# Kernel tuning notes

Measured on AMD Instinct MI355X. Metric: run time of the kernel, lower is better.

## Reference

```python
import jax, jax.numpy as jnp
import numpy as np

B, N, K, H, F_IN = 16, 2048, 8, 128, 4  # graphs, nodes/graph, knn k, hidden, input feats


def _lin(key, fi, fo):
    s = 1.0 / np.sqrt(fi)
    kw, kb = jax.random.split(key)
    W = jax.random.uniform(kw, (fi, fo), jnp.float32, -s, s)
    b = jax.random.uniform(kb, (fo,), jnp.float32, -s, s)
    return W, b


def setup_inputs() -> dict:
    key = jax.random.key(0)
    ks = jax.random.split(key, 10)
    x = jax.random.normal(ks[0], (B * N, F_IN), jnp.float32)
    edge_index = jax.random.randint(ks[1], (2, B * N * K), 0, B * N, jnp.int64)  # unused by forward
    batch = jnp.repeat(jnp.arange(B, dtype=jnp.int64), N)
    W_enc, b_enc = _lin(ks[2], F_IN, H)
    W1a, b1a = _lin(ks[3], 2 * H, H)
    W1b, b1b = _lin(ks[4], H, H)
    W2a, b2a = _lin(ks[5], 2 * H, H)
    W2b, b2b = _lin(ks[6], H, H)
    W5a, b5a = _lin(ks[7], 2 * H, H)
    W5b, b5b = _lin(ks[8], H, 1)
    return dict(x=x, edge_index=edge_index, batch=batch,
                W_enc=W_enc, b_enc=b_enc,
                W1a=W1a, b1a=b1a, W1b=W1b, b1b=b1b,
                W2a=W2a, b2a=b2a, W2b=W2b, b2b=b2b,
                W5a=W5a, b5a=b5a, W5b=W5b, b5b=b5b)


def _knn(xb):
    # xb: [N, H] -> [N, K] indices of k nearest neighbors (self included, as in torch_cluster.knn)
    sq = jnp.sum(xb * xb, axis=-1)
    d = sq[:, None] + sq[None, :] - 2.0 * (xb @ xb.T)  # squared distances [N, N]
    return jax.lax.top_k(-d, K)[1]


def _edge_conv(x, Wa, ba, Wb, bb):
    # DynamicEdgeConv: rebuild kNN on current features, message = MLP([x_i, x_j - x_i]), max-aggregate.
    idx = jax.vmap(_knn)(x)                                   # [B, N, K]
    xj = jax.vmap(lambda xb, ib: xb[ib])(x, idx)              # [B, N, K, Hin]
    xi = jnp.broadcast_to(x[:, :, None, :], xj.shape)
    e = jnp.concatenate([xi, xj - xi], axis=-1)               # [B, N, K, 2*Hin]
    h = jax.nn.relu(e @ Wa + ba)                              # MLP applies ReLU after each Linear
    h = jax.nn.relu(h @ Wb + bb)
    return jnp.max(h, axis=2)                                 # max aggregation over neighbors


def reference(x, edge_index, batch, W_enc, b_enc,
              W1a, b1a, W1b, b1b, W2a, b2a, W2b, b2b, W5a, b5a, W5b, b5b):
    # batch is contiguous equal-size graphs -> reshape; edge_index is ignored by the original forward.
    h = x.reshape(B, N, F_IN) @ W_enc + b_enc
    h = jax.nn.relu(_edge_conv(h, W1a, b1a, W1b, b1b))
    h = jax.nn.relu(_edge_conv(h, W2a, b2a, W2b, b2b))
    out = jax.nn.sigmoid(_edge_conv(h, W5a, b5a, W5b, b5b))   # note: last MLP layer also has ReLU
    return out.reshape(B * N, 1)
```

## Files before the change

### kernel.cpp

```cpp
#include <hip/hip_runtime.h>
#include <hip/hip_bf16.h>
#include <math.h>

#define BGR 16
#define NPG 2048
#define HD  128
#define KNN 8
#define NTOT (BGR*NPG)

using bf16x8 = __attribute__((ext_vector_type(8))) short;
using f32x4  = __attribute__((ext_vector_type(4))) float;
using f32x16 = __attribute__((ext_vector_type(16))) float;

typedef __attribute__((address_space(3))) unsigned int lds_uint;
typedef const __attribute__((address_space(1))) unsigned int glob_uint;
#define GLOAD_LDS16(g, l) __builtin_amdgcn_global_load_lds((glob_uint*)(g), (lds_uint*)(l), 16, 0, 0)

__device__ inline unsigned short bf16rn(float f) {
    unsigned u = __float_as_uint(f);
    unsigned r = (u + 0x7FFFu + ((u >> 16) & 1u)) >> 16;
    return (unsigned short)r;
}
__device__ inline float bf16tof(unsigned short h) {
    return __uint_as_float(((unsigned)h) << 16);
}

__device__ inline void wcat_body(const float* __restrict__ Wa,
                                 unsigned short* __restrict__ Wt, int lb, int t)
{
    int gid = lb * 256 + t;
    int k = gid >> 8, n = gid & 255;
    float w;
    if (n < 128) w = Wa[(128 + k) * 128 + n];
    else { int nn = n - 128; w = Wa[k * 128 + nn] - Wa[(128 + k) * 128 + nn]; }
    unsigned short b1 = bf16rn(w);  float r1 = w - bf16tof(b1);
    unsigned short b2 = bf16rn(r1);
    int cs = n >> 5, h = (n >> 4) & 1, c = n & 15, kc = k >> 5, kg = (k >> 3) & 3, e = k & 7;
    size_t off = (size_t)cs * 12288 + kc * 1024 + h * 512 + kg * 128 + c * 8 + e;
    Wt[off] = b1; Wt[off + 4096] = b2;
}

__device__ inline void wb_body(const float* __restrict__ Wb,
                               unsigned short* __restrict__ Wt, int lb, int t)
{
    int gid = lb * 256 + t;
    int k = gid >> 7, n = gid & 127;
    float w = Wb[k * 128 + n];
    unsigned short b1 = bf16rn(w);  float r1 = w - bf16tof(b1);
    unsigned short b2 = bf16rn(r1);
    int cs = n >> 5, h = (n >> 4) & 1, c = n & 15, kc = k >> 5, kg = (k >> 3) & 3, e = k & 7;
    size_t off = (size_t)cs * 12288 + kc * 1024 + h * 512 + kg * 128 + c * 8 + e;
    Wt[off] = b1; Wt[off + 4096] = b2;
}

__global__ __launch_bounds__(256) void setup_all(const float* __restrict__ x,
                                                 const float* __restrict__ We,
                                                 const float* __restrict__ be,
                                                 unsigned short* __restrict__ hs,
                                                 float* __restrict__ sqg,
                                                 const float* __restrict__ W1a,
                                                 const float* __restrict__ W2a,
                                                 const float* __restrict__ W5a,
                                                 const float* __restrict__ W1b,
                                                 const float* __restrict__ W2b,
                                                 unsigned short* __restrict__ Wt1,
                                                 unsigned short* __restrict__ Wt2,
                                                 unsigned short* __restrict__ Wt5,
                                                 unsigned short* __restrict__ Wbt1,
                                                 unsigned short* __restrict__ Wbt2)
{
    const int bb = blockIdx.x, t = threadIdx.x;
    if (bb < 8192) {
        const size_t plane = (size_t)NTOT * HD;
        int node = (bb * 256 + t) >> 6;
        int lane = t & 63;
        float4 xv = *(const float4*)(x + (size_t)node * 4);
        float v0 = be[lane], v1 = be[lane + 64];
        const float* xf = (const float*)&xv;
#pragma unroll
        for (int f = 0; f < 4; ++f) {
            v0 = fmaf(xf[f], We[f * 128 + lane], v0);
            v1 = fmaf(xf[f], We[f * 128 + lane + 64], v1);
        }
        float s = fmaf(v0, v0, v1 * v1);
#pragma unroll
        for (int off = 32; off >= 1; off >>= 1)
            s += __shfl_xor(s, off);
        if (lane == 0) sqg[node] = s;
#pragma unroll
        for (int q = 0; q < 2; ++q) {
            float v = q ? v1 : v0;
            int   d = lane + q * 64;
            unsigned short b1 = bf16rn(v);  float r1 = v - bf16tof(b1);
            unsigned short b2 = bf16rn(r1);
            size_t base = (size_t)node * HD + d;
            hs[base]         = b1;
            hs[base + plane] = b2;
        }
    }
    else if (bb < 8320) wcat_body(W1a, Wt1, bb - 8192, t);
    else if (bb < 8448) wcat_body(W2a, Wt2, bb - 8320, t);
    else if (bb < 8576) wcat_body(W5a, Wt5, bb - 8448, t);
    else if (bb < 8640) wb_body(W1b, Wbt1, bb - 8576, t);
    else                wb_body(W2b, Wbt2, bb - 8640, t);
}

#define THREEPASS(B00,B01,B10,B11) \
    acc0 = __builtin_amdgcn_mfma_f32_16x16x32_bf16(A0[kc], B00, acc0, 0, 0, 0); \
    acc1 = __builtin_amdgcn_mfma_f32_16x16x32_bf16(A0[kc], B01, acc1, 0, 0, 0); \
    acc0 = __builtin_amdgcn_mfma_f32_16x16x32_bf16(A1[kc], B00, acc0, 0, 0, 0); \
    acc1 = __builtin_amdgcn_mfma_f32_16x16x32_bf16(A1[kc], B01, acc1, 0, 0, 0); \
    acc0 = __builtin_amdgcn_mfma_f32_16x16x32_bf16(A0[kc], B10, acc0, 0, 0, 0); \
    acc1 = __builtin_amdgcn_mfma_f32_16x16x32_bf16(A0[kc], B11, acc1, 0, 0, 0);

#define THREEPASS_G(AA0,AA1,B00,B01,B10,B11,C0,C1) \
    C0 = __builtin_amdgcn_mfma_f32_16x16x32_bf16(AA0[kc], B00, C0, 0, 0, 0); \
    C1 = __builtin_amdgcn_mfma_f32_16x16x32_bf16(AA0[kc], B01, C1, 0, 0, 0); \
    C0 = __builtin_amdgcn_mfma_f32_16x16x32_bf16(AA1[kc], B00, C0, 0, 0, 0); \
    C1 = __builtin_amdgcn_mfma_f32_16x16x32_bf16(AA1[kc], B01, C1, 0, 0, 0); \
    C0 = __builtin_amdgcn_mfma_f32_16x16x32_bf16(AA0[kc], B10, C0, 0, 0, 0); \
    C1 = __builtin_amdgcn_mfma_f32_16x16x32_bf16(AA0[kc], B11, C1, 0, 0, 0);

#define SELECT(PA, PB, PS) { \
    const unsigned lidbase = (unsigned)((PS) << 4); \
    _Pragma("unroll") \
    for (int i = 0; i < 16; ++i) { \
        float dsum = (PA)[i] + (PB)[i]; \
        unsigned ku = (__float_as_uint(dsum) & 0xFFFFFF00u) \
                    | (lidbase + (unsigned)i); \
        float kk = __uint_as_float(ku); \
        bd[7] = __builtin_amdgcn_fmed3f(bd[6], kk, bd[7]); \
        bd[6] = __builtin_amdgcn_fmed3f(bd[5], kk, bd[6]); \
        bd[5] = __builtin_amdgcn_fmed3f(bd[4], kk, bd[5]); \
        bd[4] = __builtin_amdgcn_fmed3f(bd[3], kk, bd[4]); \
        bd[3] = __builtin_amdgcn_fmed3f(bd[2], kk, bd[3]); \
        bd[2] = __builtin_amdgcn_fmed3f(bd[1], kk, bd[2]); \
        bd[1] = __builtin_amdgcn_fmed3f(bd[0], kk, bd[1]); \
        bd[0] = fminf(bd[0], kk); \
    } }

#define KNN_MFMA_STEP(ACCA, ACCB, S) { \
    const float* qq = sqs + (S) * 32 + kh * 4; \
    f32x4 q0 = *(const f32x4*)(qq); \
    f32x4 q1 = *(const f32x4*)(qq + 8); \
    f32x4 q2 = *(const f32x4*)(qq + 16); \
    f32x4 q3 = *(const f32x4*)(qq + 24); \
    ACCA[0]=q0[0]; ACCA[1]=q0[1]; ACCA[2]=q0[2]; ACCA[3]=q0[3]; \
    ACCA[4]=q1[0]; ACCA[5]=q1[1]; ACCA[6]=q1[2]; ACCA[7]=q1[3]; \
    ACCA[8]=q2[0]; ACCA[9]=q2[1]; ACCA[10]=q2[2]; ACCA[11]=q2[3]; \
    ACCA[12]=q3[0]; ACCA[13]=q3[1]; ACCA[14]=q3[2]; ACCA[15]=q3[3]; \
    ACCB = (f32x16){0.f,0.f,0.f,0.f,0.f,0.f,0.f,0.f,0.f,0.f,0.f,0.f,0.f,0.f,0.f,0.f}; \
    const char* pstep = ldsc + cur * 16384 + lane * 16; \
    __builtin_amdgcn_s_setprio(1); \
    _Pragma("unroll") \
    for (int kch = 0; kch < 8; ++kch) { \
        bf16x8 c0 = *(const bf16x8*)(pstep + kch * 1024); \
        bf16x8 c1 = *(const bf16x8*)(pstep + 8192 + kch * 1024); \
        ACCA = __builtin_amdgcn_mfma_f32_32x32x16_bf16(c0, RB[0][kch], ACCA, 0, 0, 0); \
        ACCB = __builtin_amdgcn_mfma_f32_32x32x16_bf16(c1, RB[0][kch], ACCB, 0, 0, 0); \
        if (kch & 1) ACCA = __builtin_amdgcn_mfma_f32_32x32x16_bf16(c0, RB[1][kch], ACCA, 0, 0, 0); \
        else         ACCB = __builtin_amdgcn_mfma_f32_32x32x16_bf16(c0, RB[1][kch], ACCB, 0, 0, 0); \
    } \
    __builtin_amdgcn_s_setprio(0); }

__global__ __launch_bounds__(256, 3) void knn_node(const unsigned short* __restrict__ hs,
                                                   const float* __restrict__ sqg,
                                                   const unsigned short* __restrict__ Wt,
                                                   const float* __restrict__ ba,
                                                   float* __restrict__ P,
                                                   float* __restrict__ D,
                                                   float* __restrict__ cand_d)
{
    __shared__ ulong2 ldsraw[2176];
    char* ldsc = (char*)ldsraw;
    const size_t plane = (size_t)NTOT * HD;
    const int t = threadIdx.x;
    const int wv = t >> 6, lane = t & 63;

    if (blockIdx.x < 512) {
        const int lrow = lane & 15, kg = lane >> 4;
        const int nodebase = blockIdx.x * 64 + wv * 16;

        const unsigned short* arow = hs + (size_t)(nodebase + lrow) * HD + kg * 8;
        bf16x8 A0[4], A1[4];
#pragma unroll
        for (int kc = 0; kc < 4; ++kc) {
            A0[kc] = *(const bf16x8*)(arow + kc * 32);
            A1[kc] = *(const bf16x8*)(arow + plane + kc * 32);
        }

        char* ldsw = ldsc + wv * 1024;
        const unsigned short* wsrc = Wt + t * 8;
#pragma unroll
        for (int i = 0; i < 4; ++i)
            GLOAD_LDS16(wsrc + i * 2048, ldsw + i * 4096);
        __syncthreads();

        int cur = 0;
        for (int cs = 0; cs < 8; ++cs) {
            if (cs < 7) {
#pragma unroll
                for (int i = 0; i < 4; ++i)
                    GLOAD_LDS16(wsrc + (size_t)(cs + 1) * 12288 + i * 2048,
                                ldsc + (cur ^ 1) * 16384 + wv * 1024 + i * 4096);
            }
            const char* pb = ldsc + cur * 16384 + kg * 256 + lrow * 16;
            f32x4 acc0 = {0.f,0.f,0.f,0.f};
            f32x4 acc1 = {0.f,0.f,0.f,0.f};
#pragma unroll
            for (int kc = 0; kc < 4; ++kc) {
                const char* pk = pb + kc * 2048;
                bf16x8 b00 = *(const bf16x8*)(pk);
                bf16x8 b01 = *(const bf16x8*)(pk + 1024);
                bf16x8 b10 = *(const bf16x8*)(pk + 8192);
                bf16x8 b11 = *(const bf16x8*)(pk + 9216);
                THREEPASS(b00, b01, b10, b11)
            }
            int n0 = cs * 32 + lrow;
            if (cs < 4) {
#pragma unroll
                for (int r = 0; r < 4; ++r) {
                    size_t row = (size_t)(nodebase + kg * 4 + r) * HD;
                    P[row + n0]      = acc0[r];
                    P[row + n0 + 16] = acc1[r];
                }
            } else {
                float ba0 = ba[n0 - 128], ba1 = ba[n0 - 112];
#pragma unroll
                for (int r = 0; r < 4; ++r) {
                    size_t row = (size_t)(nodebase + kg * 4 + r) * HD;
                    D[row + n0 - 128] = acc0[r] + ba0;
                    D[row + n0 - 112] = acc1[r] + ba1;
                }
            }
            __syncthreads();
            cur ^= 1;
        }
        return;
    }

    float* sqs = (float*)(ldsc + 32768);
    const int b = blockIdx.x - 512;
    const int slot = b >> 3;
    const int g  = (b & 7) | ((slot & 1) << 3);
    const int rb = (slot >> 1) & 15;
    const int cs = (slot >> 5) & 3;
    const int gbase = g * NPG;
    const int cbase = cs * 512;
    const int rl = lane & 31, kh = lane >> 5;
    const int myrow = rb * 128 + wv * 32 + rl;

    sqs[t]       = sqg[gbase + cbase + t];
    sqs[t + 256] = sqg[gbase + cbase + 256 + t];

    bf16x8 RB[2][8];
    {
        const unsigned short* rrow = hs + (size_t)(gbase + myrow) * HD + kh * 8;
#pragma unroll
        for (int p = 0; p < 2; ++p)
#pragma unroll
            for (int kch = 0; kch < 8; ++kch) {
                bf16x8 v = *(const bf16x8*)(rrow + (size_t)p * plane + kch * 16);
                unsigned* u = (unsigned*)&v;
#pragma unroll
                for (int w = 0; w < 4; ++w)
                    u[w] = (u[w] + 0x00800080u) ^ 0x80008000u;
                RB[p][kch] = v;
            }
    }

    const unsigned short* sb = hs + (size_t)(gbase + cbase + (t & 31)) * HD
                             + (t >> 6) * 16 + ((t >> 5) & 1) * 8;

#pragma unroll
    for (int i = 0; i < 4; ++i)
        GLOAD_LDS16(sb + (size_t)(i >> 1) * plane + (i & 1) * 64,
                    ldsc + wv * 1024 + i * 4096);
    __syncthreads();

    const float INF = __uint_as_float(0x7F800000u);
    float bd[8];
#pragma unroll
    for (int s = 0; s < 8; ++s) bd[s] = INF;

    f32x16 accA, accB;
    int cur = 0;
    for (int s = 0; s < 16; ++s) {
        if (s < 15) {
            const unsigned short* sbn = sb + (size_t)(s + 1) * 32 * HD;
#pragma unroll
            for (int i = 0; i < 4; ++i)
                GLOAD_LDS16(sbn + (size_t)(i >> 1) * plane + (i & 1) * 64,
                            ldsc + (cur ^ 1) * 16384 + wv * 1024 + i * 4096);
        }
        KNN_MFMA_STEP(accA, accB, s)
        SELECT(accA, accB, s)
        __syncthreads();
        cur ^= 1;
    }

    const size_t ob = (size_t)(gbase + myrow) * 64 + cs * 16 + kh * 8;
    f32x4 o0, o1;
#pragma unroll
    for (int sel = 0; sel < 8; ++sel) {
        unsigned u = __float_as_uint(bd[sel]);
        unsigned lid = u & 255u;
        unsigned j = (unsigned)(cbase + (int)(lid >> 4) * 32 + (int)((lid >> 2) & 3u) * 8
                              + kh * 4 + (int)(lid & 3u));
        float kv = __uint_as_float((u & 0xFFFFF800u) | j);
        if (sel < 4) o0[sel] = kv; else o1[sel - 4] = kv;
    }
    *(f32x4*)(cand_d + ob)     = o0;
    *(f32x4*)(cand_d + ob + 4) = o1;
}

template<bool FINAL>
__global__ __launch_bounds__(256) void edge_mlp(const float* __restrict__ P,
                                                const float* __restrict__ D,
                                                const float* __restrict__ cand_d,
                                                const unsigned short* __restrict__ Wbt,
                                                const float* __restrict__ bb,
                                                const float* __restrict__ w5,
                                                unsigned short* __restrict__ hsout,
                                                float* __restrict__ sqgout,
                                                float* __restrict__ out)
{
    __shared__ ulong2 ldsraw[2112];
    char* lds = (char*)ldsraw;
    int* nbrs = (int*)(lds + 32768);
    const size_t plane = (size_t)NTOT * HD;
    const int t = threadIdx.x, wv = t >> 6, lane = t & 63;
    const int lrow = lane & 15, kg = lane >> 4;
    const int node0 = blockIdx.x * 16;
    const int bn = node0 + wv * 4;

    char* ldsw = lds + wv * 1024;
    const unsigned short* wsrc = Wbt + t * 8;
    if (!FINAL) {
#pragma unroll
        for (int i = 0; i < 4; ++i)
            GLOAD_LDS16(wsrc + i * 2048, ldsw + i * 4096);
    }

    if (t < 128) {
        const int row = node0 + (t >> 3);
        const int run = t & 7;
        const int gb = (row >> 11) << 11;
        const float* pd = cand_d + (size_t)row * 64 + run * 8;
        float d[8];
#pragma unroll
        for (int k = 0; k < 8; ++k) d[k] = pd[k];
        const float INF = __uint_as_float(0x7F800000u);
        float hd = d[0];
#pragma unroll
        for (int sel = 0; sel < 8; ++sel) {
            float md = hd;
#pragma unroll
            for (int m = 1; m < 8; m <<= 1)
                md = fminf(md, __shfl_xor(md, m, 8));
            if (run == sel)
                nbrs[(t >> 3) * 8 + sel] = gb + (int)(__float_as_uint(md) & 0x7FFu);
            bool win = (hd == md);
            if (win) {
                d[0]=d[1]; d[1]=d[2]; d[2]=d[3]; d[3]=d[4];
                d[4]=d[5]; d[5]=d[6]; d[6]=d[7]; d[7]=INF;
            }
            hd = d[0];
        }
    }
    __syncthreads();

    const int en = lrow >> 3;
    const int ee = lrow & 7;
    const int i0 = bn + en;
    const int i1 = bn + 2 + en;
    const int j0 = nbrs[(wv * 4 + en) * 8 + ee];
    const int j1 = nbrs[(wv * 4 + 2 + en) * 8 + ee];

    const float* dp0 = D + (size_t)i0 * HD + kg * 8;
    const float* pp0 = P + (size_t)j0 * HD + kg * 8;
    const float* dp1 = D + (size_t)i1 * HD + kg * 8;
    const float* pp1 = P + (size_t)j1 * HD + kg * 8;

    bf16x8 A0a[4], A1a[4], A0b[4], A1b[4];
    float sdot0 = 0.f, sdot1 = 0.f;
#pragma unroll
    for (int kc = 0; kc < 4; ++kc) {
#pragma unroll
        for (int gsel = 0; gsel < 2; ++gsel) {
            const float* dpx = gsel ? dp1 : dp0;
            const float* ppx = gsel ? pp1 : pp0;
            float4 d0 = *(const float4*)(dpx + kc * 32);
            float4 d1 = *(const float4*)(dpx + kc * 32 + 4);
            float4 p0 = *(const float4*)(ppx + kc * 32);
            float4 p1 = *(const float4*)(ppx + kc * 32 + 4);
            float v[8];
            v[0]=fmaxf(d0.x+p0.x,0.f); v[1]=fmaxf(d0.y+p0.y,0.f);
            v[2]=fmaxf(d0.z+p0.z,0.f); v[3]=fmaxf(d0.w+p0.w,0.f);
            v[4]=fmaxf(d1.x+p1.x,0.f); v[5]=fmaxf(d1.y+p1.y,0.f);
            v[6]=fmaxf(d1.z+p1.z,0.f); v[7]=fmaxf(d1.w+p1.w,0.f);
            if (FINAL) {
                float s = 0.f;
#pragma unroll
                for (int e = 0; e < 8; ++e)
                    s = fmaf(v[e], w5[kc * 32 + kg * 8 + e], s);
                if (gsel) sdot1 += s; else sdot0 += s;
            } else {
#pragma unroll
                for (int e = 0; e < 8; ++e) {
                    unsigned short b1 = bf16rn(v[e]); float r1 = v[e] - bf16tof(b1);
                    unsigned short b2 = bf16rn(r1);
                    if (gsel) { A0b[kc][e] = (short)b1; A1b[kc][e] = (short)b2; }
                    else      { A0a[kc][e] = (short)b1; A1a[kc][e] = (short)b2; }
                }
            }
        }
    }

    if (!FINAL) {
        const bool writer = (kg & 1) == 0;
        const int mn0 = bn + (kg >> 1);
        const int mn1 = bn + 2 + (kg >> 1);
        float sqacc0 = 0.f, sqacc1 = 0.f;

        int cur = 0;
        for (int cs = 0; cs < 4; ++cs) {
            if (cs < 3) {
#pragma unroll
                for (int i = 0; i < 4; ++i)
                    GLOAD_LDS16(wsrc + (size_t)(cs + 1) * 12288 + i * 2048,
                                lds + (cur ^ 1) * 16384 + wv * 1024 + i * 4096);
            }
            const char* pb = lds + cur * 16384 + kg * 256 + lrow * 16;
            f32x4 acc0a = {0.f,0.f,0.f,0.f}, acc1a = {0.f,0.f,0.f,0.f};
            f32x4 acc0b = {0.f,0.f,0.f,0.f}, acc1b = {0.f,0.f,0.f,0.f};
#pragma unroll
            for (int kc = 0; kc < 4; ++kc) {
                const char* pk = pb + kc * 2048;
                bf16x8 b00 = *(const bf16x8*)(pk);
                bf16x8 b01 = *(const bf16x8*)(pk + 1024);
                bf16x8 b10 = *(const bf16x8*)(pk + 8192);
                bf16x8 b11 = *(const bf16x8*)(pk + 9216);
                THREEPASS_G(A0a, A1a, b00, b01, b10, b11, acc0a, acc1a)
                THREEPASS_G(A0b, A1b, b00, b01, b10, b11, acc0b, acc1b)
            }
            float bb0 = bb[cs * 32 + lrow];
            float bb1 = bb[cs * 32 + 16 + lrow];
            {
                float m0 = fmaxf(fmaxf(acc0a[0], acc0a[1]), fmaxf(acc0a[2], acc0a[3]));
                float m1 = fmaxf(fmaxf(acc1a[0], acc1a[1]), fmaxf(acc1a[2], acc1a[3]));
                m0 = fmaxf(m0 + bb0, 0.f);
                m1 = fmaxf(m1 + bb1, 0.f);
                m0 = fmaxf(m0, __shfl_xor(m0, 16));
                m1 = fmaxf(m1, __shfl_xor(m1, 16));
                if (writer) {
                    sqacc0 = fmaf(m0, m0, fmaf(m1, m1, sqacc0));
                    size_t base = (size_t)mn0 * HD + cs * 32 + lrow;
                    unsigned short c1 = bf16rn(m0); float r1 = m0 - bf16tof(c1);
                    unsigned short c2 = bf16rn(r1);
                    hsout[base]         = c1;
                    hsout[base + plane] = c2;
                    unsigned short e1 = bf16rn(m1); float s1 = m1 - bf16tof(e1);
                    unsigned short e2 = bf16rn(s1);
                    hsout[base + 16]         = e1;
                    hsout[base + 16 + plane] = e2;
                }
            }
            {
                float m0 = fmaxf(fmaxf(acc0b[0], acc0b[1]), fmaxf(acc0b[2], acc0b[3]));
                float m1 = fmaxf(fmaxf(acc1b[0], acc1b[1]), fmaxf(acc1b[2], acc1b[3]));
                m0 = fmaxf(m0 + bb0, 0.f);
                m1 = fmaxf(m1 + bb1, 0.f);
                m0 = fmaxf(m0, __shfl_xor(m0, 16));
                m1 = fmaxf(m1, __shfl_xor(m1, 16));
                if (writer) {
                    sqacc1 = fmaf(m0, m0, fmaf(m1, m1, sqacc1));
                    size_t base = (size_t)mn1 * HD + cs * 32 + lrow;
                    unsigned short c1 = bf16rn(m0); float r1 = m0 - bf16tof(c1);
                    unsigned short c2 = bf16rn(r1);
                    hsout[base]         = c1;
                    hsout[base + plane] = c2;
                    unsigned short e1 = bf16rn(m1); float s1 = m1 - bf16tof(e1);
                    unsigned short e2 = bf16rn(s1);
                    hsout[base + 16]         = e1;
                    hsout[base + 16 + plane] = e2;
                }
            }
            __syncthreads();
            cur ^= 1;
        }
        if (writer) {
#pragma unroll
            for (int m = 1; m < 16; m <<= 1) {
                sqacc0 += __shfl_xor(sqacc0, m, 16);
                sqacc1 += __shfl_xor(sqacc1, m, 16);
            }
            if (lrow == 0) {
                sqgout[mn0] = sqacc0;
                sqgout[mn1] = sqacc1;
            }
        }
    } else {
        sdot0 += __shfl_xor(sdot0, 16);
        sdot0 += __shfl_xor(sdot0, 32);
        sdot1 += __shfl_xor(sdot1, 16);
        sdot1 += __shfl_xor(sdot1, 32);
        float s0 = fmaxf(sdot0 + bb[0], 0.f);
        float s1 = fmaxf(sdot1 + bb[0], 0.f);
#pragma unroll
        for (int m = 1; m < 8; m <<= 1) {
            s0 = fmaxf(s0, __shfl_xor(s0, m));
            s1 = fmaxf(s1, __shfl_xor(s1, m));
        }
        if (lane == 0) {
            out[bn]     = 1.f / (1.f + expf(-s0));
            out[bn + 2] = 1.f / (1.f + expf(-s1));
        }
        if (lane == 8) {
            out[bn + 1] = 1.f / (1.f + expf(-s0));
            out[bn + 3] = 1.f / (1.f + expf(-s1));
        }
    }
}

extern "C" void kernel_launch(void* const* d_in, const int* in_sizes, int n_in,
                              void* d_out, int out_size, void* d_ws, size_t ws_size,
                              hipStream_t stream) {
    const float* x     = (const float*)d_in[0];
    const float* W_enc = (const float*)d_in[3];
    const float* b_enc = (const float*)d_in[4];
    const float* W1a = (const float*)d_in[5];
    const float* b1a = (const float*)d_in[6];
    const float* W1b = (const float*)d_in[7];
    const float* b1b = (const float*)d_in[8];
    const float* W2a = (const float*)d_in[9];
    const float* b2a = (const float*)d_in[10];
    const float* W2b = (const float*)d_in[11];
    const float* b2b = (const float*)d_in[12];
    const float* W5a = (const float*)d_in[13];
    const float* b5a = (const float*)d_in[14];
    const float* W5b = (const float*)d_in[15];
    const float* b5b = (const float*)d_in[16];

    unsigned short* hs = (unsigned short*)d_ws;
    float* sqg  = (float*)(hs + (size_t)2*NTOT*HD);
    float* cd   = sqg + NTOT;
    float* Dbuf = cd + (size_t)NTOT*64;
    float* Pbuf = Dbuf + (size_t)NTOT*HD;
    unsigned short* Wt1  = (unsigned short*)(Pbuf + (size_t)NTOT*HD);
    unsigned short* Wt2  = Wt1 + 98304;
    unsigned short* Wt5  = Wt2 + 98304;
    unsigned short* Wbt1 = Wt5 + 98304;
    unsigned short* Wbt2 = Wbt1 + 49152;

    setup_all<<<8704, 256, 0, stream>>>(x, W_enc, b_enc, hs, sqg,
                                        W1a, W2a, W5a, W1b, W2b,
                                        Wt1, Wt2, Wt5, Wbt1, Wbt2);

    knn_node<<<1536, 256, 0, stream>>>(hs, sqg, Wt1, b1a, Pbuf, Dbuf, cd);
    edge_mlp<false><<<NTOT/16, 256, 0, stream>>>(Pbuf, Dbuf, cd, Wbt1, b1b, nullptr, hs, sqg, nullptr);

    knn_node<<<1536, 256, 0, stream>>>(hs, sqg, Wt2, b2a, Pbuf, Dbuf, cd);
    edge_mlp<false><<<NTOT/16, 256, 0, stream>>>(Pbuf, Dbuf, cd, Wbt2, b2b, nullptr, hs, sqg, nullptr);

    knn_node<<<1536, 256, 0, stream>>>(hs, sqg, Wt5, b5a, Pbuf, Dbuf, cd);
    edge_mlp<true><<<NTOT/16, 256, 0, stream>>>(Pbuf, Dbuf, cd, nullptr, b5b, W5b, nullptr, nullptr, (float*)d_out);
}
```

Before: 304.6 us.

## Triple-buffer kNN candidate tiles with prefetch distance two and partial vmcnt waits

The kNN distance loop moves from double to triple LDS buffering. Candidate tiles are prefetched two steps ahead, and the full __syncthreads is replaced with an explicit s_waitcnt vmcnt(4) plus s_barrier, so one tile's loads can stay in flight across each barrier. This is meant to hide global-to-LDS latency behind the MFMA and selection work. LDS use per block rises from about 34KB to about 51KB, which may reduce occupancy under launch_bounds(256,3).

Result: no change. 310.3 us (+1.9%).

```diff
diff --git a/kernel.cpp b/kernel.cpp
--- a/kernel.cpp
+++ b/kernel.cpp
@@ -139,7 +139,7 @@
         bd[0] = fminf(bd[0], kk); \
     } }
 
-#define KNN_MFMA_STEP(ACCA, ACCB, S) { \
+#define KNN_MFMA_STEP(ACCA, ACCB, S, BOFF) { \
     const float* qq = sqs + (S) * 32 + kh * 4; \
     f32x4 q0 = *(const f32x4*)(qq); \
     f32x4 q1 = *(const f32x4*)(qq + 8); \
@@ -150,7 +150,7 @@
     ACCA[8]=q2[0]; ACCA[9]=q2[1]; ACCA[10]=q2[2]; ACCA[11]=q2[3]; \
     ACCA[12]=q3[0]; ACCA[13]=q3[1]; ACCA[14]=q3[2]; ACCA[15]=q3[3]; \
     ACCB = (f32x16){0.f,0.f,0.f,0.f,0.f,0.f,0.f,0.f,0.f,0.f,0.f,0.f,0.f,0.f,0.f,0.f}; \
-    const char* pstep = ldsc + cur * 16384 + lane * 16; \
+    const char* pstep = ldsc + (BOFF) + lane * 16; \
     __builtin_amdgcn_s_setprio(1); \
     _Pragma("unroll") \
     for (int kch = 0; kch < 8; ++kch) { \
@@ -171,7 +171,7 @@
                                                    float* __restrict__ D,
                                                    float* __restrict__ cand_d)
 {
-    __shared__ ulong2 ldsraw[2176];
+    __shared__ ulong2 ldsraw[3200];
     char* ldsc = (char*)ldsraw;
     const size_t plane = (size_t)NTOT * HD;
     const int t = threadIdx.x;
@@ -239,7 +239,7 @@
         return;
     }
 
-    float* sqs = (float*)(ldsc + 32768);
+    float* sqs = (float*)(ldsc + 49152);
     const int b = blockIdx.x - 512;
     const int slot = b >> 3;
     const int g  = (b & 7) | ((slot & 1) << 3);
@@ -276,7 +276,16 @@
     for (int i = 0; i < 4; ++i)
         GLOAD_LDS16(sb + (size_t)(i >> 1) * plane + (i & 1) * 64,
                     ldsc + wv * 1024 + i * 4096);
-    __syncthreads();
+    {
+        const unsigned short* sb1 = sb + (size_t)32 * HD;
+#pragma unroll
+        for (int i = 0; i < 4; ++i)
+            GLOAD_LDS16(sb1 + (size_t)(i >> 1) * plane + (i & 1) * 64,
+                        ldsc + 16384 + wv * 1024 + i * 4096);
+    }
+    asm volatile("s_waitcnt vmcnt(4) lgkmcnt(0)" ::: "memory");
+    __builtin_amdgcn_sched_barrier(0);
+    __builtin_amdgcn_s_barrier();
 
     const float INF = __uint_as_float(0x7F800000u);
     float bd[8];
@@ -284,19 +293,24 @@
     for (int s = 0; s < 8; ++s) bd[s] = INF;
 
     f32x16 accA, accB;
-    int cur = 0;
+    int c0 = 0, c2 = 2;
     for (int s = 0; s < 16; ++s) {
-        if (s < 15) {
-            const unsigned short* sbn = sb + (size_t)(s + 1) * 32 * HD;
+        if (s < 14) {
+            const unsigned short* sbn = sb + (size_t)(s + 2) * 32 * HD;
+            const int boff = c2 * 16384 + wv * 1024;
 #pragma unroll
             for (int i = 0; i < 4; ++i)
                 GLOAD_LDS16(sbn + (size_t)(i >> 1) * plane + (i & 1) * 64,
-                            ldsc + (cur ^ 1) * 16384 + wv * 1024 + i * 4096);
-        }
-        KNN_MFMA_STEP(accA, accB, s)
+                            ldsc + boff + i * 4096);
+        }
+        KNN_MFMA_STEP(accA, accB, s, c0 * 16384)
         SELECT(accA, accB, s)
-        __syncthreads();
-        cur ^= 1;
+        if (s < 14) asm volatile("s_waitcnt vmcnt(4)" ::: "memory");
+        else        asm volatile("s_waitcnt vmcnt(0)" ::: "memory");
+        __builtin_amdgcn_sched_barrier(0);
+        __builtin_amdgcn_s_barrier();
+        c0 = (c0 == 2) ? 0 : c0 + 1;
+        c2 = (c2 == 2) ? 0 : c2 + 1;
     }
 
     const size_t ob = (size_t)(gbase + myrow) * 64 + cs * 16 + kh * 8;
```
